# Optimization experiments

Hardware: AMD Instinct MI355X
Metric: run time of the kernel (lower is better)

Reference implementation:

```python
import jax, jax.numpy as jnp
import numpy as np

B, NQ, NKV = 16, 4096, 77
QUERY_DIM, CONTEXT_DIM = 320, 768
HEADS, DIM_HEAD = 8, 64
INNER = HEADS * DIM_HEAD
SCALE = DIM_HEAD ** (-0.5)
MAX_NEG = -jnp.finfo(jnp.float32).max / 2


def setup_inputs() -> dict:
    key = jax.random.key(0)
    ks = jax.random.split(key, 8)
    x = jax.random.normal(ks[0], (B, NQ, QUERY_DIM), dtype=jnp.float32)
    context = jax.random.normal(ks[1], (B, NKV, CONTEXT_DIM), dtype=jnp.float32)
    mask = jax.random.randint(ks[2], (B, 1, 1, NKV), 0, 2).astype(bool)
    s = 0.02
    Wq = jax.random.normal(ks[3], (QUERY_DIM, INNER), dtype=jnp.float32) * s
    Wk = jax.random.normal(ks[4], (CONTEXT_DIM, INNER), dtype=jnp.float32) * s
    Wv = jax.random.normal(ks[5], (CONTEXT_DIM, INNER), dtype=jnp.float32) * s
    Wo = jax.random.normal(ks[6], (INNER, QUERY_DIM), dtype=jnp.float32) * s
    bo = jnp.zeros((QUERY_DIM,), dtype=jnp.float32)
    return {"x": x, "context": context, "mask": mask,
            "Wq": Wq, "Wk": Wk, "Wv": Wv, "Wo": Wo, "bo": bo}


def reference(x, context, mask, Wq, Wk, Wv, Wo, bo):
    # projections (bias-free Linears)
    q = (x @ Wq).reshape(B, NQ, HEADS, DIM_HEAD)        # b q h d
    k = (context @ Wk).reshape(B, NKV, HEADS, DIM_HEAD)  # b k h d
    v = (context @ Wv).reshape(B, NKV, HEADS, DIM_HEAD)  # b k h d
    # additive mask bias: 0 where mask, -finfo.max/2 where ~mask (matches masked_fill_)
    bias = jnp.where(mask, jnp.float32(0), MAX_NEG)      # broadcast to b h q k
    sim = jnp.einsum('bqhd,bkhd->bhqk', q, k) * SCALE + bias
    attn = jax.nn.softmax(sim, axis=-1)
    out = jnp.einsum('bhqk,bkhd->bqhd', attn, v).reshape(B, NQ, INNER)
    return out @ Wo + bo  # dropout p=0 -> identity
```

## Files before the change

### kernel.cpp

```cpp
#include <hip/hip_runtime.h>

typedef unsigned short ushort_t;
typedef __attribute__((ext_vector_type(8))) short bf16x8;
typedef __attribute__((ext_vector_type(4))) float f32x4;

#define B_SZ   16
#define NQ     4096
#define NKV    77
#define QDIM   320
#define CDIM   768
#define HEADS  8
#define DHEAD  64
#define INNER  512
#define M_ROWS (B_SZ * NQ)
#define VT_STR 104

__device__ __forceinline__ ushort_t f2bf(float f) {
  unsigned u = __builtin_bit_cast(unsigned, f);
  u = (u + 0x7fffu + ((u >> 16) & 1u)) >> 16;
  return (ushort_t)u;
}

__device__ __forceinline__ void async16(const ushort_t* g, ushort_t* l) {
  __builtin_amdgcn_global_load_lds(
      (const __attribute__((address_space(1))) unsigned int*)g,
      (__attribute__((address_space(3))) unsigned int*)l,
      16, 0, 0);
}

__device__ __forceinline__ bf16x8 cvt8(f32x4 lo, f32x4 hi) {
  unsigned w0, w1, w2, w3;
  asm("v_cvt_pk_bf16_f32 %0, %1, %2" : "=v"(w0) : "v"(lo[0]), "v"(lo[1]));
  asm("v_cvt_pk_bf16_f32 %0, %1, %2" : "=v"(w1) : "v"(lo[2]), "v"(lo[3]));
  asm("v_cvt_pk_bf16_f32 %0, %1, %2" : "=v"(w2) : "v"(hi[0]), "v"(hi[1]));
  asm("v_cvt_pk_bf16_f32 %0, %1, %2" : "=v"(w3) : "v"(hi[2]), "v"(hi[3]));
  union { unsigned u[4]; bf16x8 v; } cv;
  cv.u[0] = w0; cv.u[1] = w1; cv.u[2] = w2; cv.u[3] = w3;
  return cv.v;
}

#define VMCNT(N) asm volatile("s_waitcnt vmcnt(" #N ")" ::: "memory")

__global__ void mask_bias_kernel(const unsigned char* __restrict__ mraw,
                                 float* __restrict__ biasT) {
  __shared__ int s_u8, s_w4;
  if (threadIdx.x == 0) { s_u8 = 0; s_w4 = 0; }
  __syncthreads();
  const int nbytes = B_SZ * NKV;
  for (int i = threadIdx.x; i < nbytes; i += blockDim.x) {
    unsigned char v = mraw[i];
    if (v && (i & 3)) atomicOr(&s_u8, 1);
    if (v && ((i & 7) == 4)) atomicOr(&s_w4, 1);
  }
  __syncthreads();
  int mode = s_u8 ? 0 : (s_w4 ? 1 : 2);
  for (int i = threadIdx.x; i < B_SZ * 80; i += blockDim.x) {
    int b = i / 80, kv = i - b * 80;
    float bias = -2e30f;
    if (kv < NKV) {
      int idx = b * NKV + kv;
      long long m;
      if (mode == 0)      m = (long long)mraw[idx];
      else if (mode == 1) m = (long long)((const int*)mraw)[idx];
      else                m = ((const long long*)mraw)[idx];
      bias = m ? 0.0f : -1e30f;
    }
    biasT[i] = bias;
  }
}

#define PREP_T0 236544
#define PREP_T1 400384
#define PREP_T2 1186816
#define PREP_T3 1383424
__global__ void prep_kernel(const float* __restrict__ ctx, ushort_t* __restrict__ cb,
                            const float* __restrict__ Wq, ushort_t* __restrict__ Wqb,
                            const float* __restrict__ Wk, const float* __restrict__ Wv,
                            ushort_t* __restrict__ Wkvb,
                            const float* __restrict__ Wo, ushort_t* __restrict__ Wob) {
  int i = blockIdx.x * blockDim.x + threadIdx.x;
  const int stride = gridDim.x * blockDim.x;
  for (; i < PREP_T3; i += stride) {
    if (i < PREP_T0) {
      float4 v = ((const float4*)ctx)[i];
      ushort4 o;
      o.x = f2bf(v.x); o.y = f2bf(v.y); o.z = f2bf(v.z); o.w = f2bf(v.w);
      ((ushort4*)cb)[i] = o;
    } else if (i < PREP_T1) {
      int j = i - PREP_T0;
      int n = j / QDIM, k = j - n * QDIM;
      Wqb[j] = f2bf(Wq[(size_t)k * INNER + n] * 0.125f);
    } else if (i < PREP_T2) {
      int j = i - PREP_T1;
      int n = j / CDIM, k = j - n * CDIM;
      float v = (n < INNER) ? Wk[(size_t)k * INNER + n]
                            : Wv[(size_t)k * INNER + (n - INNER)];
      Wkvb[j] = f2bf(v);
    } else {
      int j = i - PREP_T2;
      int n = j / INNER, k = j - n * INNER;
      Wob[j] = (n < QDIM) ? f2bf(Wo[(size_t)k * QDIM + n]) : (ushort_t)0;
    }
  }
}

__global__ __launch_bounds__(256) void gemm_bf16(
    const ushort_t* __restrict__ A, const ushort_t* __restrict__ Bt,
    ushort_t* __restrict__ Cb,
    int K, int Astride, int Bstride, int Cstride) {
  __shared__ ushort_t As[128 * 64];
  __shared__ ushort_t Bs[128 * 64];
  const int tid = threadIdx.x;
  const int wid = tid >> 6, lane = tid & 63;
  const int wr = wid >> 1, wc = wid & 1;
  const int tileM = blockIdx.x * 128, tileN = blockIdx.y * 128;

  f32x4 acc[4][4];
#pragma unroll
  for (int m = 0; m < 4; ++m)
#pragma unroll
    for (int n = 0; n < 4; ++n) acc[m][n] = (f32x4){0.f, 0.f, 0.f, 0.f};

  const int srow = lane >> 3;
  const int scol = (lane & 7) * 8;

  for (int kt = 0; kt < K; kt += 64) {
    __syncthreads();
#pragma unroll
    for (int j = 0; j < 4; ++j) {
      int s = wid * 4 + j;
      const ushort_t* ga = A + (size_t)(tileM + s * 8 + srow) * Astride + kt + scol;
      const ushort_t* gb = Bt + (size_t)(tileN + s * 8 + srow) * Bstride + kt + scol;
      async16(ga, As + s * 512);
      async16(gb, Bs + s * 512);
    }
    __syncthreads();
#pragma unroll
    for (int kc = 0; kc < 2; ++kc) {
      bf16x8 af[4], bfr[4];
#pragma unroll
      for (int m = 0; m < 4; ++m)
        af[m] = *(const bf16x8*)&As[(wr * 64 + m * 16 + (lane & 15)) * 64 + kc * 32 + (lane >> 4) * 8];
#pragma unroll
      for (int n = 0; n < 4; ++n)
        bfr[n] = *(const bf16x8*)&Bs[(wc * 64 + n * 16 + (lane & 15)) * 64 + kc * 32 + (lane >> 4) * 8];
#pragma unroll
      for (int m = 0; m < 4; ++m)
#pragma unroll
        for (int n = 0; n < 4; ++n)
          acc[m][n] = __builtin_amdgcn_mfma_f32_16x16x32_bf16(af[m], bfr[n], acc[m][n], 0, 0, 0);
    }
  }

  const int r0 = tileM + wr * 64;
  const int c0 = tileN + wc * 64;
  const int rl2 = (lane >> 4) * 4;
  const int cl = lane & 15;
#pragma unroll
  for (int m = 0; m < 4; ++m)
#pragma unroll
    for (int n = 0; n < 4; ++n) {
      int col = c0 + n * 16 + cl;
#pragma unroll
      for (int r = 0; r < 4; ++r)
        Cb[(size_t)(r0 + m * 16 + rl2 + r) * Cstride + col] = f2bf(acc[m][n][r]);
    }
}

__global__ void vtrans_kernel(const ushort_t* __restrict__ kvb,
                              ushort_t* __restrict__ vt) {
  const int h = blockIdx.y, b = blockIdx.z;
  const int wid = threadIdx.x >> 6, lane = threadIdx.x & 63;
  const int d = blockIdx.x * 4 + wid;
  ushort_t* dst = vt + (size_t)(b * HEADS + h) * (64 * VT_STR) + d * VT_STR;
  for (int kv = lane; kv < VT_STR; kv += 64)
    dst[kv] = (kv < NKV)
        ? kvb[(size_t)(b * NKV + kv) * 1024 + 512 + h * 64 + d]
        : (ushort_t)0;
}

__global__ __launch_bounds__(512, 2) void gemm_qproj_p(
    const float* __restrict__ x, const ushort_t* __restrict__ Wt,
    ushort_t* __restrict__ qb) {
  extern __shared__ char sm[];
  const int tid = threadIdx.x, wid = tid >> 6, lane = tid & 63;
  const int rl = lane & 15, g = lane >> 4;
  const int wr = wid & 1, wc = wid >> 1;
  const size_t Mbase = (size_t)blockIdx.x * 128;

  size_t asrc[2]; unsigned adst[2];
#pragma unroll
  for (int i = 0; i < 2; ++i) {
    int c = tid + i * 512, row = c >> 3, c16 = c & 7;
    asrc[i] = (Mbase + row) * 1280 + (unsigned)((c16 * 16) ^ ((row & 7) << 4));
    adst[i] = c * 16;
  }
  size_t bsrc[4]; unsigned bdst[4];
#pragma unroll
  for (int i = 0; i < 4; ++i) {
    int c = tid + i * 512, row = c >> 2, c16 = c & 3;
    bsrc[i] = (size_t)row * 640 + (unsigned)((c16 * 16) ^ ((row & 3) << 4));
    bdst[i] = 16384 + c * 16;
  }
  const char* xB = (const char*)x;
  const char* WtB = (const char*)Wt;

  f32x4 acc[4][8];
#pragma unroll
  for (int m = 0; m < 4; ++m)
#pragma unroll
    for (int n = 0; n < 8; ++n) acc[m][n] = (f32x4){0.f, 0.f, 0.f, 0.f};

#define QSTAGE(K)                                                           \
  {                                                                         \
    char* bb = sm + (unsigned)((K) % 3) * 49152u;                           \
    _Pragma("unroll")                                                       \
    for (int i = 0; i < 2; ++i)                                             \
      async16((const ushort_t*)(xB + asrc[i] + (size_t)(K) * 128),          \
              (ushort_t*)(bb + adst[i]));                                   \
    _Pragma("unroll")                                                       \
    for (int i = 0; i < 4; ++i)                                             \
      async16((const ushort_t*)(WtB + bsrc[i] + (size_t)(K) * 64),          \
              (ushort_t*)(bb + bdst[i]));                                   \
  }

  QSTAGE(0)
  QSTAGE(1)
  for (int s = 0; s < 10; ++s) {
    if (s < 8) QSTAGE(s + 2)
    if (s < 8)       { VMCNT(12); }
    else if (s == 8) { VMCNT(6); }
    else             { VMCNT(0); }
    __builtin_amdgcn_sched_barrier(0);
    __builtin_amdgcn_s_barrier();
    __builtin_amdgcn_sched_barrier(0);

    const char* Ab = sm + (unsigned)(s % 3) * 49152u;
    const char* Bb = Ab + 16384;
    bf16x8 af[4], bfr[8];
#pragma unroll
    for (int m = 0; m < 4; ++m) {
      const int row = wr * 64 + m * 16 + rl;
      const int sw = (row & 7) << 4;
      f32x4 lo = *(const f32x4*)(Ab + row * 128 + ((g * 32) ^ sw));
      f32x4 hi = *(const f32x4*)(Ab + row * 128 + ((g * 32 + 16) ^ sw));
      af[m] = cvt8(lo, hi);
    }
#pragma unroll
    for (int n = 0; n < 8; ++n) {
      const int row = wc * 128 + n * 16 + rl;
      bfr[n] = *(const bf16x8*)(Bb + row * 64 + ((g * 16) ^ ((row & 3) << 4)));
    }
#pragma unroll
    for (int m = 0; m < 4; ++m)
#pragma unroll
      for (int n = 0; n < 8; ++n)
        acc[m][n] = __builtin_amdgcn_mfma_f32_16x16x32_bf16(af[m], bfr[n], acc[m][n], 0, 0, 0);
    __builtin_amdgcn_sched_barrier(0);
    __builtin_amdgcn_s_barrier();
    __builtin_amdgcn_sched_barrier(0);
  }

  ushort_t* eb = (ushort_t*)sm;
#pragma unroll
  for (int h = 0; h < 2; ++h) {
    if (h) __syncthreads();
    if (wr == h) {
#pragma unroll
      for (int m = 0; m < 4; ++m)
#pragma unroll
        for (int n = 0; n < 8; ++n)
#pragma unroll
          for (int r = 0; r < 4; ++r)
            eb[(m * 16 + g * 4 + r) * 512 + wc * 128 + n * 16 + rl] = f2bf(acc[m][n][r]);
    }
    __syncthreads();
#pragma unroll
    for (int i = 0; i < 8; ++i) {
      int c = tid + i * 512, row = c >> 6;
      *(bf16x8*)(qb + (Mbase + h * 64 + row) * 512 + (c & 63) * 8) =
          *(const bf16x8*)(eb + c * 8);
    }
  }
}

__global__ __launch_bounds__(512, 2) void gemm_oproj_p(
    const ushort_t* __restrict__ A, const ushort_t* __restrict__ Wt,
    const float* __restrict__ bo, float* __restrict__ out) {
  extern __shared__ char sm[];
  const int tid = threadIdx.x, wid = tid >> 6, lane = tid & 63;
  const int rl = lane & 15, g = lane >> 4;
  const int wr = wid & 1, wc = wid >> 1;
  const size_t Mbase = (size_t)blockIdx.x * 128;

  size_t asrc; unsigned adst;
  {
    int c = tid, row = c >> 2, c16 = c & 3;
    asrc = (Mbase + row) * 1024 + (unsigned)((c16 * 16) ^ ((row & 3) << 4));
    adst = c * 16;
  }
  size_t bsrc[3]; unsigned bdst[3];
#pragma unroll
  for (int i = 0; i < 3; ++i) {
    int c = tid + i * 512, row = c >> 2, c16 = c & 3;
    bsrc[i] = (size_t)row * 1024 + (unsigned)((c16 * 16) ^ ((row & 3) << 4));
    bdst[i] = 8192 + c * 16;
  }
  const char* AB = (const char*)A;
  const char* WtB = (const char*)Wt;

  f32x4 acc[4][6];
#pragma unroll
  for (int m = 0; m < 4; ++m)
#pragma unroll
    for (int n = 0; n < 6; ++n) acc[m][n] = (f32x4){0.f, 0.f, 0.f, 0.f};

#define OSTAGE(K)                                                           \
  {                                                                         \
    char* bb = sm + (unsigned)((K) % 3) * 32768u;                           \
    async16((const ushort_t*)(AB + asrc + (size_t)(K) * 64),                \
            (ushort_t*)(bb + adst));                                        \
    _Pragma("unroll")                                                       \
    for (int i = 0; i < 3; ++i)                                             \
      async16((const ushort_t*)(WtB + bsrc[i] + (size_t)(K) * 64),          \
              (ushort_t*)(bb + bdst[i]));                                   \
  }

  OSTAGE(0)
  OSTAGE(1)
  for (int s = 0; s < 16; ++s) {
    if (s < 14) OSTAGE(s + 2)
    if (s < 14)       { VMCNT(8); }
    else if (s == 14) { VMCNT(4); }
    else              { VMCNT(0); }
    __builtin_amdgcn_sched_barrier(0);
    __builtin_amdgcn_s_barrier();
    __builtin_amdgcn_sched_barrier(0);

    const char* Ab = sm + (unsigned)(s % 3) * 32768u;
    const char* Bb = Ab + 8192;
    bf16x8 af[4], bfr[6];
#pragma unroll
    for (int m = 0; m < 4; ++m) {
      const int row = wr * 64 + m * 16 + rl;
      af[m] = *(const bf16x8*)(Ab + row * 64 + ((g * 16) ^ ((row & 3) << 4)));
    }
#pragma unroll
    for (int n = 0; n < 6; ++n) {
      const int row = wc * 96 + n * 16 + rl;
      bfr[n] = *(const bf16x8*)(Bb + row * 64 + ((g * 16) ^ ((row & 3) << 4)));
    }
#pragma unroll
    for (int m = 0; m < 4; ++m)
#pragma unroll
      for (int n = 0; n < 6; ++n)
        acc[m][n] = __builtin_amdgcn_mfma_f32_16x16x32_bf16(af[m], bfr[n], acc[m][n], 0, 0, 0);
    __builtin_amdgcn_sched_barrier(0);
    __builtin_amdgcn_s_barrier();
    __builtin_amdgcn_sched_barrier(0);
  }

  const size_t r0 = Mbase + wr * 64;
  const int c0 = wc * 96;
#pragma unroll
  for (int n = 0; n < 6; ++n) {
    int col = c0 + n * 16 + rl;
    if (col < QDIM) {
      float bv = bo[col];
#pragma unroll
      for (int m = 0; m < 4; ++m)
#pragma unroll
        for (int r = 0; r < 4; ++r)
          out[(r0 + m * 16 + g * 4 + r) * QDIM + col] = acc[m][n][r] + bv;
    }
  }
}

__global__ __launch_bounds__(256) void attn_kernel(
    const ushort_t* __restrict__ qb, const ushort_t* __restrict__ kvb,
    const ushort_t* __restrict__ vt, const float* __restrict__ biasT,
    ushort_t* __restrict__ ab) {
  __shared__ ushort_t Vt[64 * VT_STR];
  __shared__ ushort_t P[4 * 16 * VT_STR];
  const int qt = blockIdx.x, h = blockIdx.y, b = blockIdx.z;
  const int tid = threadIdx.x, wid = tid >> 6, lane = tid & 63;
  const int rl = lane & 15;
  const int kh = (lane >> 4) * 8;

  const ushort_t* vtg = vt + (size_t)(b * HEADS + h) * (64 * VT_STR);
  for (int i = tid; i < 832; i += 256) async16(vtg + i * 8, Vt + i * 8);
  for (int i = tid; i < 832; i += 256)
    *(bf16x8*)&P[i * 8] = (bf16x8){0, 0, 0, 0, 0, 0, 0, 0};

  bf16x8 kf[5][2];
  float bias_v[5];
#pragma unroll
  for (int nt = 0; nt < 5; ++nt) {
    int kv = nt * 16 + rl;
    bias_v[nt] = biasT[b * 80 + kv];
    kf[nt][0] = (bf16x8){0, 0, 0, 0, 0, 0, 0, 0};
    kf[nt][1] = (bf16x8){0, 0, 0, 0, 0, 0, 0, 0};
    if (kv < NKV) {
      const ushort_t* kp = &kvb[(size_t)(b * NKV + kv) * 1024 + h * 64 + kh];
      kf[nt][0] = *(const bf16x8*)kp;
      kf[nt][1] = *(const bf16x8*)(kp + 32);
    }
  }
  __syncthreads();

  const int qbase = b * NQ + qt * 256;
  const int pbase = wid * (16 * VT_STR);
#pragma unroll 1
  for (int chunk = 0; chunk < 4; ++chunk) {
    if (chunk) __syncthreads();
    const int row0 = chunk * 64 + wid * 16;

    const ushort_t* qp = &qb[(size_t)(qbase + row0 + rl) * INNER + h * 64 + kh];
    bf16x8 qf0 = *(const bf16x8*)qp;
    bf16x8 qf1 = *(const bf16x8*)(qp + 32);

    f32x4 s[5];
#pragma unroll
    for (int nt = 0; nt < 5; ++nt) {
      s[nt] = (f32x4){0.f, 0.f, 0.f, 0.f};
      s[nt] = __builtin_amdgcn_mfma_f32_16x16x32_bf16(qf0, kf[nt][0], s[nt], 0, 0, 0);
      s[nt] = __builtin_amdgcn_mfma_f32_16x16x32_bf16(qf1, kf[nt][1], s[nt], 0, 0, 0);
    }

    float mx[4] = {-3.0e38f, -3.0e38f, -3.0e38f, -3.0e38f};
#pragma unroll
    for (int nt = 0; nt < 5; ++nt)
#pragma unroll
      for (int r = 0; r < 4; ++r) {
        float v = s[nt][r] + bias_v[nt];
        s[nt][r] = v;
        mx[r] = fmaxf(mx[r], v);
      }
#pragma unroll
    for (int d = 1; d < 16; d <<= 1)
#pragma unroll
      for (int r = 0; r < 4; ++r) mx[r] = fmaxf(mx[r], __shfl_xor(mx[r], d, 64));

    float sm_[4] = {0.f, 0.f, 0.f, 0.f};
#pragma unroll
    for (int nt = 0; nt < 5; ++nt)
#pragma unroll
      for (int r = 0; r < 4; ++r) {
        float p = __expf(s[nt][r] - mx[r]);
        s[nt][r] = p;
        sm_[r] += p;
      }
#pragma unroll
    for (int d = 1; d < 16; d <<= 1)
#pragma unroll
      for (int r = 0; r < 4; ++r) sm_[r] += __shfl_xor(sm_[r], d, 64);

    float rcp[4];
#pragma unroll
    for (int r = 0; r < 4; ++r) rcp[r] = 1.0f / sm_[r];

#pragma unroll
    for (int nt = 0; nt < 5; ++nt)
#pragma unroll
      for (int r = 0; r < 4; ++r)
        P[pbase + ((lane >> 4) * 4 + r) * VT_STR + nt * 16 + rl] = f2bf(s[nt][r]);

    f32x4 o[4];
#pragma unroll
    for (int n = 0; n < 4; ++n) o[n] = (f32x4){0.f, 0.f, 0.f, 0.f};
#pragma unroll
    for (int kc = 0; kc < 3; ++kc) {
      bf16x8 pf = *(const bf16x8*)&P[pbase + rl * VT_STR + kc * 32 + kh];
#pragma unroll
      for (int n = 0; n < 4; ++n) {
        bf16x8 vf = *(const bf16x8*)&Vt[(n * 16 + rl) * VT_STR + kc * 32 + kh];
        o[n] = __builtin_amdgcn_mfma_f32_16x16x32_bf16(pf, vf, o[n], 0, 0, 0);
      }
    }

#pragma unroll
    for (int n = 0; n < 4; ++n)
#pragma unroll
      for (int r = 0; r < 4; ++r)
        P[pbase + ((lane >> 4) * 4 + r) * VT_STR + n * 16 + rl] = f2bf(o[n][r] * rcp[r]);

    __syncthreads();

    {
      const int rflat = tid >> 2, d0 = (tid & 3) * 16;
      const ushort_t* src = &P[(rflat >> 4) * (16 * VT_STR) + (rflat & 15) * VT_STR + d0];
      ushort_t* dst = &ab[(size_t)(qbase + chunk * 64 + rflat) * INNER + h * 64 + d0];
      *(bf16x8*)dst = *(const bf16x8*)src;
      *(bf16x8*)(dst + 8) = *(const bf16x8*)(src + 8);
    }
  }
}

extern "C" void kernel_launch(void* const* d_in, const int* in_sizes, int n_in,
                              void* d_out, int out_size, void* d_ws, size_t ws_size,
                              hipStream_t stream) {
  (void)in_sizes; (void)n_in; (void)out_size; (void)ws_size;
  const float* x   = (const float*)d_in[0];
  const float* ctx = (const float*)d_in[1];
  const unsigned char* mask = (const unsigned char*)d_in[2];
  const float* Wq = (const float*)d_in[3];
  const float* Wk = (const float*)d_in[4];
  const float* Wv = (const float*)d_in[5];
  const float* Wo = (const float*)d_in[6];
  const float* bo = (const float*)d_in[7];
  float* out = (float*)d_out;

  hipFuncSetAttribute((const void*)gemm_qproj_p,
                      hipFuncAttributeMaxDynamicSharedMemorySize, 147456);
  hipFuncSetAttribute((const void*)gemm_oproj_p,
                      hipFuncAttributeMaxDynamicSharedMemorySize, 98304);

  char* ws = (char*)d_ws;
  size_t off = 0;
  auto alloc = [&](size_t bytes) {
    char* p = ws + off;
    off += (bytes + 255) & ~(size_t)255;
    return p;
  };
  float*    biasT = (float*)alloc(B_SZ * 80 * sizeof(float));
  ushort_t* ab    = (ushort_t*)alloc((size_t)M_ROWS * INNER * 2);
  ushort_t* qb    = (ushort_t*)alloc((size_t)M_ROWS * INNER * 2);
  ushort_t* cb    = (ushort_t*)alloc((size_t)1280 * CDIM * 2);
  ushort_t* Wqb   = (ushort_t*)alloc((size_t)INNER * QDIM * 2);
  ushort_t* Wkvb  = (ushort_t*)alloc((size_t)1024 * CDIM * 2);
  ushort_t* Wob   = (ushort_t*)alloc((size_t)384 * INNER * 2);
  ushort_t* kvb   = (ushort_t*)alloc((size_t)1280 * 1024 * 2);
  ushort_t* vt    = (ushort_t*)alloc((size_t)B_SZ * HEADS * 64 * VT_STR * 2);

  mask_bias_kernel<<<1, 256, 0, stream>>>(mask, biasT);
  prep_kernel<<<2048, 256, 0, stream>>>(ctx, cb, Wq, Wqb, Wk, Wv, Wkvb, Wo, Wob);

  gemm_qproj_p<<<M_ROWS / 128, 512, 147456, stream>>>(x, Wqb, qb);
  dim3 g2(1280 / 128, 1024 / 128);
  gemm_bf16<<<g2, 256, 0, stream>>>(cb, Wkvb, kvb, CDIM, CDIM, CDIM, 1024);
  vtrans_kernel<<<dim3(16, HEADS, B_SZ), 256, 0, stream>>>(kvb, vt);
  attn_kernel<<<dim3(NQ / 256, HEADS, B_SZ), 256, 0, stream>>>(qb, kvb, vt, biasT, ab);
  gemm_oproj_p<<<M_ROWS / 128, 512, 98304, stream>>>(ab, Wob, bo, out);
}
```

Before: 182.7 us.

## Pre-convert x to bf16 in prep kernel and fold mask bias into it

The prep kernel now also converts the full fp32 x activation to a bf16 buffer and computes the mask bias in block 0, which removes the separate mask kernel launch. The Q-projection GEMM reads the bf16 copy directly, halving its A-tile loads and shared-memory footprint and dropping the in-loop fp32-to-bf16 conversion. The cost is an extra full pass over x: it is read in fp32 and written in bf16, then read again by the GEMM. Total memory traffic for x therefore grows, and so does workspace use.

After: 189.5 us. 1.04x slower.

```diff
diff --git a/kernel.cpp b/kernel.cpp
--- a/kernel.cpp
+++ b/kernel.cpp
@@ -28,64 +28,61 @@
       16, 0, 0);
 }
 
-__device__ __forceinline__ bf16x8 cvt8(f32x4 lo, f32x4 hi) {
-  unsigned w0, w1, w2, w3;
-  asm("v_cvt_pk_bf16_f32 %0, %1, %2" : "=v"(w0) : "v"(lo[0]), "v"(lo[1]));
-  asm("v_cvt_pk_bf16_f32 %0, %1, %2" : "=v"(w1) : "v"(lo[2]), "v"(lo[3]));
-  asm("v_cvt_pk_bf16_f32 %0, %1, %2" : "=v"(w2) : "v"(hi[0]), "v"(hi[1]));
-  asm("v_cvt_pk_bf16_f32 %0, %1, %2" : "=v"(w3) : "v"(hi[2]), "v"(hi[3]));
-  union { unsigned u[4]; bf16x8 v; } cv;
-  cv.u[0] = w0; cv.u[1] = w1; cv.u[2] = w2; cv.u[3] = w3;
-  return cv.v;
-}
-
 #define VMCNT(N) asm volatile("s_waitcnt vmcnt(" #N ")" ::: "memory")
 
-__global__ void mask_bias_kernel(const unsigned char* __restrict__ mraw,
-                                 float* __restrict__ biasT) {
-  __shared__ int s_u8, s_w4;
-  if (threadIdx.x == 0) { s_u8 = 0; s_w4 = 0; }
-  __syncthreads();
-  const int nbytes = B_SZ * NKV;
-  for (int i = threadIdx.x; i < nbytes; i += blockDim.x) {
-    unsigned char v = mraw[i];
-    if (v && (i & 3)) atomicOr(&s_u8, 1);
-    if (v && ((i & 7) == 4)) atomicOr(&s_w4, 1);
-  }
-  __syncthreads();
-  int mode = s_u8 ? 0 : (s_w4 ? 1 : 2);
-  for (int i = threadIdx.x; i < B_SZ * 80; i += blockDim.x) {
-    int b = i / 80, kv = i - b * 80;
-    float bias = -2e30f;
-    if (kv < NKV) {
-      int idx = b * NKV + kv;
-      long long m;
-      if (mode == 0)      m = (long long)mraw[idx];
-      else if (mode == 1) m = (long long)((const int*)mraw)[idx];
-      else                m = ((const long long*)mraw)[idx];
-      bias = m ? 0.0f : -1e30f;
-    }
-    biasT[i] = bias;
-  }
-}
-
-#define PREP_T0 236544
-#define PREP_T1 400384
-#define PREP_T2 1186816
-#define PREP_T3 1383424
-__global__ void prep_kernel(const float* __restrict__ ctx, ushort_t* __restrict__ cb,
+#define PREP_X  5242880
+#define PREP_T0 (PREP_X + 236544)
+#define PREP_T1 (PREP_T0 + 163840)
+#define PREP_T2 (PREP_T1 + 786432)
+#define PREP_T3 (PREP_T2 + 196608)
+__global__ void prep_kernel(const float* __restrict__ x, ushort_t* __restrict__ xb,
+                            const float* __restrict__ ctx, ushort_t* __restrict__ cb,
                             const float* __restrict__ Wq, ushort_t* __restrict__ Wqb,
                             const float* __restrict__ Wk, const float* __restrict__ Wv,
                             ushort_t* __restrict__ Wkvb,
-                            const float* __restrict__ Wo, ushort_t* __restrict__ Wob) {
+                            const float* __restrict__ Wo, ushort_t* __restrict__ Wob,
+                            const unsigned char* __restrict__ mraw,
+                            float* __restrict__ biasT) {
+  if (blockIdx.x == 0) {
+    __shared__ int s_u8, s_w4;
+    if (threadIdx.x == 0) { s_u8 = 0; s_w4 = 0; }
+    __syncthreads();
+    const int nbytes = B_SZ * NKV;
+    for (int i = threadIdx.x; i < nbytes; i += blockDim.x) {
+      unsigned char v = mraw[i];
+      if (v && (i & 3)) atomicOr(&s_u8, 1);
+      if (v && ((i & 7) == 4)) atomicOr(&s_w4, 1);
+    }
+    __syncthreads();
+    int mode = s_u8 ? 0 : (s_w4 ? 1 : 2);
+    for (int i = threadIdx.x; i < B_SZ * 80; i += blockDim.x) {
+      int b = i / 80, kv = i - b * 80;
+      float bias = -2e30f;
+      if (kv < NKV) {
+        int idx = b * NKV + kv;
+        long long m;
+        if (mode == 0)      m = (long long)mraw[idx];
+        else if (mode == 1) m = (long long)((const int*)mraw)[idx];
+        else                m = ((const long long*)mraw)[idx];
+        bias = m ? 0.0f : -1e30f;
+      }
+      biasT[i] = bias;
+    }
+  }
   int i = blockIdx.x * blockDim.x + threadIdx.x;
   const int stride = gridDim.x * blockDim.x;
   for (; i < PREP_T3; i += stride) {
-    if (i < PREP_T0) {
-      float4 v = ((const float4*)ctx)[i];
+    if (i < PREP_X) {
+      float4 v = ((const float4*)x)[i];
       ushort4 o;
       o.x = f2bf(v.x); o.y = f2bf(v.y); o.z = f2bf(v.z); o.w = f2bf(v.w);
-      ((ushort4*)cb)[i] = o;
+      ((ushort4*)xb)[i] = o;
+    } else if (i < PREP_T0) {
+      int j = i - PREP_X;
+      float4 v = ((const float4*)ctx)[j];
+      ushort4 o;
+      o.x = f2bf(v.x); o.y = f2bf(v.y); o.z = f2bf(v.z); o.w = f2bf(v.w);
+      ((ushort4*)cb)[j] = o;
     } else if (i < PREP_T1) {
       int j = i - PREP_T0;
       int n = j / QDIM, k = j - n * QDIM;
@@ -179,8 +176,8 @@
         : (ushort_t)0;
 }
 
-__global__ __launch_bounds__(512, 2) void gemm_qproj_p(
-    const float* __restrict__ x, const ushort_t* __restrict__ Wt,
+__global__ __launch_bounds__(512, 2) void gemm_qproj_o(
+    const ushort_t* __restrict__ A, const ushort_t* __restrict__ Wt,
     ushort_t* __restrict__ qb) {
   extern __shared__ char sm[];
   const int tid = threadIdx.x, wid = tid >> 6, lane = tid & 63;
@@ -188,21 +185,20 @@
   const int wr = wid & 1, wc = wid >> 1;
   const size_t Mbase = (size_t)blockIdx.x * 128;
 
-  size_t asrc[2]; unsigned adst[2];
-#pragma unroll
-  for (int i = 0; i < 2; ++i) {
-    int c = tid + i * 512, row = c >> 3, c16 = c & 7;
-    asrc[i] = (Mbase + row) * 1280 + (unsigned)((c16 * 16) ^ ((row & 7) << 4));
-    adst[i] = c * 16;
+  size_t asrc; unsigned adst;
+  {
+    int c = tid, row = c >> 2, c16 = c & 3;
+    asrc = (Mbase + row) * 640 + (unsigned)((c16 * 16) ^ ((row & 3) << 4));
+    adst = c * 16;
   }
   size_t bsrc[4]; unsigned bdst[4];
 #pragma unroll
   for (int i = 0; i < 4; ++i) {
     int c = tid + i * 512, row = c >> 2, c16 = c & 3;
     bsrc[i] = (size_t)row * 640 + (unsigned)((c16 * 16) ^ ((row & 3) << 4));
-    bdst[i] = 16384 + c * 16;
-  }
-  const char* xB = (const char*)x;
+    bdst[i] = 8192 + c * 16;
+  }
+  const char* AB = (const char*)A;
   const char* WtB = (const char*)Wt;
 
   f32x4 acc[4][8];
@@ -211,40 +207,35 @@
 #pragma unroll
     for (int n = 0; n < 8; ++n) acc[m][n] = (f32x4){0.f, 0.f, 0.f, 0.f};
 
-#define QSTAGE(K)                                                           \
+#define QSTAGE2(K)                                                          \
   {                                                                         \
-    char* bb = sm + (unsigned)((K) % 3) * 49152u;                           \
-    _Pragma("unroll")                                                       \
-    for (int i = 0; i < 2; ++i)                                             \
-      async16((const ushort_t*)(xB + asrc[i] + (size_t)(K) * 128),          \
-              (ushort_t*)(bb + adst[i]));                                   \
+    char* bb = sm + (unsigned)((K) % 3) * 40960u;                           \
+    async16((const ushort_t*)(AB + asrc + (size_t)(K) * 64),                \
+            (ushort_t*)(bb + adst));                                        \
     _Pragma("unroll")                                                       \
     for (int i = 0; i < 4; ++i)                                             \
       async16((const ushort_t*)(WtB + bsrc[i] + (size_t)(K) * 64),          \
               (ushort_t*)(bb + bdst[i]));                                   \
   }
 
-  QSTAGE(0)
-  QSTAGE(1)
+  QSTAGE2(0)
+  QSTAGE2(1)
   for (int s = 0; s < 10; ++s) {
-    if (s < 8) QSTAGE(s + 2)
-    if (s < 8)       { VMCNT(12); }
-    else if (s == 8) { VMCNT(6); }
+    if (s < 8) QSTAGE2(s + 2)
+    if (s < 8)       { VMCNT(10); }
+    else if (s == 8) { VMCNT(5); }
     else             { VMCNT(0); }
     __builtin_amdgcn_sched_barrier(0);
     __builtin_amdgcn_s_barrier();
     __builtin_amdgcn_sched_barrier(0);
 
-    const char* Ab = sm + (unsigned)(s % 3) * 49152u;
-    const char* Bb = Ab + 16384;
+    const char* Ab = sm + (unsigned)(s % 3) * 40960u;
+    const char* Bb = Ab + 8192;
     bf16x8 af[4], bfr[8];
 #pragma unroll
     for (int m = 0; m < 4; ++m) {
       const int row = wr * 64 + m * 16 + rl;
-      const int sw = (row & 7) << 4;
-      f32x4 lo = *(const f32x4*)(Ab + row * 128 + ((g * 32) ^ sw));
-      f32x4 hi = *(const f32x4*)(Ab + row * 128 + ((g * 32 + 16) ^ sw));
-      af[m] = cvt8(lo, hi);
+      af[m] = *(const bf16x8*)(Ab + row * 64 + ((g * 16) ^ ((row & 3) << 4)));
     }
 #pragma unroll
     for (int n = 0; n < 8; ++n) {
@@ -510,8 +501,8 @@
   const float* bo = (const float*)d_in[7];
   float* out = (float*)d_out;
 
-  hipFuncSetAttribute((const void*)gemm_qproj_p,
-                      hipFuncAttributeMaxDynamicSharedMemorySize, 147456);
+  hipFuncSetAttribute((const void*)gemm_qproj_o,
+                      hipFuncAttributeMaxDynamicSharedMemorySize, 122880);
   hipFuncSetAttribute((const void*)gemm_oproj_p,
                       hipFuncAttributeMaxDynamicSharedMemorySize, 98304);
 
@@ -525,6 +516,7 @@
   float*    biasT = (float*)alloc(B_SZ * 80 * sizeof(float));
   ushort_t* ab    = (ushort_t*)alloc((size_t)M_ROWS * INNER * 2);
   ushort_t* qb    = (ushort_t*)alloc((size_t)M_ROWS * INNER * 2);
+  ushort_t* xb    = (ushort_t*)alloc((size_t)M_ROWS * QDIM * 2);
   ushort_t* cb    = (ushort_t*)alloc((size_t)1280 * CDIM * 2);
   ushort_t* Wqb   = (ushort_t*)alloc((size_t)INNER * QDIM * 2);
   ushort_t* Wkvb  = (ushort_t*)alloc((size_t)1024 * CDIM * 2);
@@ -532,10 +524,10 @@
   ushort_t* kvb   = (ushort_t*)alloc((size_t)1280 * 1024 * 2);
   ushort_t* vt    = (ushort_t*)alloc((size_t)B_SZ * HEADS * 64 * VT_STR * 2);
 
-  mask_bias_kernel<<<1, 256, 0, stream>>>(mask, biasT);
-  prep_kernel<<<2048, 256, 0, stream>>>(ctx, cb, Wq, Wqb, Wk, Wv, Wkvb, Wo, Wob);
-
-  gemm_qproj_p<<<M_ROWS / 128, 512, 147456, stream>>>(x, Wqb, qb);
+  prep_kernel<<<2048, 256, 0, stream>>>(x, xb, ctx, cb, Wq, Wqb,
+                                        Wk, Wv, Wkvb, Wo, Wob, mask, biasT);
+
+  gemm_qproj_o<<<M_ROWS / 128, 512, 122880, stream>>>(xb, Wqb, qb);
   dim3 g2(1280 / 128, 1024 / 128);
   gemm_bf16<<<g2, 256, 0, stream>>>(cb, Wkvb, kvb, CDIM, CDIM, CDIM, 1024);
   vtrans_kernel<<<dim3(16, HEADS, B_SZ), 256, 0, stream>>>(kvb, vt);
```

## Split Q projection GEMM into 128x128 output tiles over a 2D grid

Applied to the files above, without the earlier changes.

The Q-projection kernel now computes 128x128 output tiles on a (4, M/128) grid instead of full 128x512 row panels. This cuts LDS per block and accumulator registers, allowing more resident blocks and more parallelism. The cost is that each x row tile, stored in fp32, is loaded and converted to bf16 four times, which raises global/L2 traffic. The epilogue is simplified to a single padded LDS staging pass.

Result: slower. 198.1 us (+8.4%).

```diff
diff --git a/kernel.cpp b/kernel.cpp
--- a/kernel.cpp
+++ b/kernel.cpp
@@ -179,14 +179,15 @@
         : (ushort_t)0;
 }
 
-__global__ __launch_bounds__(512, 2) void gemm_qproj_p(
+__global__ __launch_bounds__(512, 2) void gemm_qproj_f(
     const float* __restrict__ x, const ushort_t* __restrict__ Wt,
     ushort_t* __restrict__ qb) {
   extern __shared__ char sm[];
   const int tid = threadIdx.x, wid = tid >> 6, lane = tid & 63;
   const int rl = lane & 15, g = lane >> 4;
   const int wr = wid & 1, wc = wid >> 1;
-  const size_t Mbase = (size_t)blockIdx.x * 128;
+  const int Nbase = blockIdx.x * 128;
+  const size_t Mbase = (size_t)blockIdx.y * 128;
 
   size_t asrc[2]; unsigned adst[2];
 #pragma unroll
@@ -195,49 +196,45 @@
     asrc[i] = (Mbase + row) * 1280 + (unsigned)((c16 * 16) ^ ((row & 7) << 4));
     adst[i] = c * 16;
   }
-  size_t bsrc[4]; unsigned bdst[4];
-#pragma unroll
-  for (int i = 0; i < 4; ++i) {
-    int c = tid + i * 512, row = c >> 2, c16 = c & 3;
-    bsrc[i] = (size_t)row * 640 + (unsigned)((c16 * 16) ^ ((row & 3) << 4));
-    bdst[i] = 16384 + c * 16;
+  size_t bsrc; unsigned bdst;
+  {
+    int row = tid >> 2, c16 = tid & 3;
+    bsrc = (size_t)(Nbase + row) * 640 + (unsigned)((c16 * 16) ^ ((row & 3) << 4));
+    bdst = 16384 + tid * 16;
   }
   const char* xB = (const char*)x;
   const char* WtB = (const char*)Wt;
 
-  f32x4 acc[4][8];
+  f32x4 acc[4][2];
 #pragma unroll
   for (int m = 0; m < 4; ++m)
 #pragma unroll
-    for (int n = 0; n < 8; ++n) acc[m][n] = (f32x4){0.f, 0.f, 0.f, 0.f};
-
-#define QSTAGE(K)                                                           \
+    for (int n = 0; n < 2; ++n) acc[m][n] = (f32x4){0.f, 0.f, 0.f, 0.f};
+
+#define FSTG(K)                                                             \
   {                                                                         \
-    char* bb = sm + (unsigned)((K) % 3) * 49152u;                           \
+    char* bb = sm + (unsigned)((K) % 3) * 24576u;                           \
     _Pragma("unroll")                                                       \
     for (int i = 0; i < 2; ++i)                                             \
       async16((const ushort_t*)(xB + asrc[i] + (size_t)(K) * 128),          \
               (ushort_t*)(bb + adst[i]));                                   \
-    _Pragma("unroll")                                                       \
-    for (int i = 0; i < 4; ++i)                                             \
-      async16((const ushort_t*)(WtB + bsrc[i] + (size_t)(K) * 64),          \
-              (ushort_t*)(bb + bdst[i]));                                   \
-  }
-
-  QSTAGE(0)
-  QSTAGE(1)
+    async16((const ushort_t*)(WtB + bsrc + (size_t)(K) * 64),               \
+            (ushort_t*)(bb + bdst));                                        \
+  }
+
+  FSTG(0)
+  FSTG(1)
   for (int s = 0; s < 10; ++s) {
-    if (s < 8) QSTAGE(s + 2)
-    if (s < 8)       { VMCNT(12); }
-    else if (s == 8) { VMCNT(6); }
+    if (s < 8)       { FSTG(s + 2) VMCNT(6); }
+    else if (s == 8) { VMCNT(3); }
     else             { VMCNT(0); }
     __builtin_amdgcn_sched_barrier(0);
     __builtin_amdgcn_s_barrier();
     __builtin_amdgcn_sched_barrier(0);
 
-    const char* Ab = sm + (unsigned)(s % 3) * 49152u;
+    const char* Ab = sm + (unsigned)(s % 3) * 24576u;
     const char* Bb = Ab + 16384;
-    bf16x8 af[4], bfr[8];
+    bf16x8 af[4], bfr[2];
 #pragma unroll
     for (int m = 0; m < 4; ++m) {
       const int row = wr * 64 + m * 16 + rl;
@@ -247,40 +244,35 @@
       af[m] = cvt8(lo, hi);
     }
 #pragma unroll
-    for (int n = 0; n < 8; ++n) {
-      const int row = wc * 128 + n * 16 + rl;
+    for (int n = 0; n < 2; ++n) {
+      const int row = wc * 32 + n * 16 + rl;
       bfr[n] = *(const bf16x8*)(Bb + row * 64 + ((g * 16) ^ ((row & 3) << 4)));
     }
 #pragma unroll
     for (int m = 0; m < 4; ++m)
 #pragma unroll
-      for (int n = 0; n < 8; ++n)
+      for (int n = 0; n < 2; ++n)
         acc[m][n] = __builtin_amdgcn_mfma_f32_16x16x32_bf16(af[m], bfr[n], acc[m][n], 0, 0, 0);
     __builtin_amdgcn_sched_barrier(0);
     __builtin_amdgcn_s_barrier();
     __builtin_amdgcn_sched_barrier(0);
   }
 
+  __syncthreads();
   ushort_t* eb = (ushort_t*)sm;
 #pragma unroll
-  for (int h = 0; h < 2; ++h) {
-    if (h) __syncthreads();
-    if (wr == h) {
-#pragma unroll
-      for (int m = 0; m < 4; ++m)
-#pragma unroll
-        for (int n = 0; n < 8; ++n)
-#pragma unroll
-          for (int r = 0; r < 4; ++r)
-            eb[(m * 16 + g * 4 + r) * 512 + wc * 128 + n * 16 + rl] = f2bf(acc[m][n][r]);
-    }
-    __syncthreads();
-#pragma unroll
-    for (int i = 0; i < 8; ++i) {
-      int c = tid + i * 512, row = c >> 6;
-      *(bf16x8*)(qb + (Mbase + h * 64 + row) * 512 + (c & 63) * 8) =
-          *(const bf16x8*)(eb + c * 8);
-    }
+  for (int m = 0; m < 4; ++m)
+#pragma unroll
+    for (int n = 0; n < 2; ++n)
+#pragma unroll
+      for (int r = 0; r < 4; ++r)
+        eb[(wr * 64 + m * 16 + g * 4 + r) * 136 + wc * 32 + n * 16 + rl] = f2bf(acc[m][n][r]);
+  __syncthreads();
+#pragma unroll
+  for (int i = 0; i < 4; ++i) {
+    int c = tid + i * 512, row = c >> 4, c8 = c & 15;
+    *(bf16x8*)(qb + (Mbase + row) * 512 + Nbase + c8 * 8) =
+        *(const bf16x8*)(eb + row * 136 + c8 * 8);
   }
 }
 
@@ -510,8 +502,8 @@
   const float* bo = (const float*)d_in[7];
   float* out = (float*)d_out;
 
-  hipFuncSetAttribute((const void*)gemm_qproj_p,
-                      hipFuncAttributeMaxDynamicSharedMemorySize, 147456);
+  hipFuncSetAttribute((const void*)gemm_qproj_f,
+                      hipFuncAttributeMaxDynamicSharedMemorySize, 73728);
   hipFuncSetAttribute((const void*)gemm_oproj_p,
                       hipFuncAttributeMaxDynamicSharedMemorySize, 98304);
 
@@ -535,7 +527,7 @@
   mask_bias_kernel<<<1, 256, 0, stream>>>(mask, biasT);
   prep_kernel<<<2048, 256, 0, stream>>>(ctx, cb, Wq, Wqb, Wk, Wv, Wkvb, Wo, Wob);
 
-  gemm_qproj_p<<<M_ROWS / 128, 512, 147456, stream>>>(x, Wqb, qb);
+  gemm_qproj_f<<<dim3(4, M_ROWS / 128), 512, 73728, stream>>>(x, Wqb, qb);
   dim3 g2(1280 / 128, 1024 / 128);
   gemm_bf16<<<g2, 256, 0, stream>>>(cb, Wkvb, kvb, CDIM, CDIM, CDIM, 1024);
   vtrans_kernel<<<dim3(16, HEADS, B_SZ), 256, 0, stream>>>(kvb, vt);
```

## Switch projection GEMMs from triple-buffered vmcnt pipeline to double buffering

Applied to the files above, without the earlier changes.

The Q-projection and output-projection GEMMs drop their three-stage async global-to-LDS pipeline, which used explicit vmcnt waits and raw s_barriers. They now use two buffers: each iteration prefetches one stage ahead and ends with __syncthreads. This cuts dynamic LDS from 144KB to 96KB for the Q projection and from 96KB to 64KB for the output projection, so the output GEMM could fit two blocks per CU. The cost is a shorter prefetch distance and a full barrier plus memory drain every iteration, which may expose more load latency.

After: 180.3 us. Within noise of the previous version (-1.3%).

```diff
diff --git a/kernel.cpp b/kernel.cpp
--- a/kernel.cpp
+++ b/kernel.cpp
@@ -38,8 +38,6 @@
   cv.u[0] = w0; cv.u[1] = w1; cv.u[2] = w2; cv.u[3] = w3;
   return cv.v;
 }
-
-#define VMCNT(N) asm volatile("s_waitcnt vmcnt(" #N ")" ::: "memory")
 
 __global__ void mask_bias_kernel(const unsigned char* __restrict__ mraw,
                                  float* __restrict__ biasT) {
@@ -213,7 +211,7 @@
 
 #define QSTAGE(K)                                                           \
   {                                                                         \
-    char* bb = sm + (unsigned)((K) % 3) * 49152u;                           \
+    char* bb = sm + (unsigned)((K) & 1) * 49152u;                           \
     _Pragma("unroll")                                                       \
     for (int i = 0; i < 2; ++i)                                             \
       async16((const ushort_t*)(xB + asrc[i] + (size_t)(K) * 128),          \
@@ -225,17 +223,11 @@
   }
 
   QSTAGE(0)
-  QSTAGE(1)
+  __syncthreads();
   for (int s = 0; s < 10; ++s) {
-    if (s < 8) QSTAGE(s + 2)
-    if (s < 8)       { VMCNT(12); }
-    else if (s == 8) { VMCNT(6); }
-    else             { VMCNT(0); }
-    __builtin_amdgcn_sched_barrier(0);
-    __builtin_amdgcn_s_barrier();
-    __builtin_amdgcn_sched_barrier(0);
-
-    const char* Ab = sm + (unsigned)(s % 3) * 49152u;
+    if (s < 9) QSTAGE(s + 1)
+
+    const char* Ab = sm + (unsigned)(s & 1) * 49152u;
     const char* Bb = Ab + 16384;
     bf16x8 af[4], bfr[8];
 #pragma unroll
@@ -256,9 +248,8 @@
 #pragma unroll
       for (int n = 0; n < 8; ++n)
         acc[m][n] = __builtin_amdgcn_mfma_f32_16x16x32_bf16(af[m], bfr[n], acc[m][n], 0, 0, 0);
-    __builtin_amdgcn_sched_barrier(0);
-    __builtin_amdgcn_s_barrier();
-    __builtin_amdgcn_sched_barrier(0);
+
+    __syncthreads();
   }
 
   ushort_t* eb = (ushort_t*)sm;
@@ -317,7 +308,7 @@
 
 #define OSTAGE(K)                                                           \
   {                                                                         \
-    char* bb = sm + (unsigned)((K) % 3) * 32768u;                           \
+    char* bb = sm + (unsigned)((K) & 1) * 32768u;                           \
     async16((const ushort_t*)(AB + asrc + (size_t)(K) * 64),                \
             (ushort_t*)(bb + adst));                                        \
     _Pragma("unroll")                                                       \
@@ -327,17 +318,11 @@
   }
 
   OSTAGE(0)
-  OSTAGE(1)
+  __syncthreads();
   for (int s = 0; s < 16; ++s) {
-    if (s < 14) OSTAGE(s + 2)
-    if (s < 14)       { VMCNT(8); }
-    else if (s == 14) { VMCNT(4); }
-    else              { VMCNT(0); }
-    __builtin_amdgcn_sched_barrier(0);
-    __builtin_amdgcn_s_barrier();
-    __builtin_amdgcn_sched_barrier(0);
-
-    const char* Ab = sm + (unsigned)(s % 3) * 32768u;
+    if (s < 15) OSTAGE(s + 1)
+
+    const char* Ab = sm + (unsigned)(s & 1) * 32768u;
     const char* Bb = Ab + 8192;
     bf16x8 af[4], bfr[6];
 #pragma unroll
@@ -355,9 +340,8 @@
 #pragma unroll
       for (int n = 0; n < 6; ++n)
         acc[m][n] = __builtin_amdgcn_mfma_f32_16x16x32_bf16(af[m], bfr[n], acc[m][n], 0, 0, 0);
-    __builtin_amdgcn_sched_barrier(0);
-    __builtin_amdgcn_s_barrier();
-    __builtin_amdgcn_sched_barrier(0);
+
+    __syncthreads();
   }
 
   const size_t r0 = Mbase + wr * 64;
@@ -511,9 +495,9 @@
   float* out = (float*)d_out;
 
   hipFuncSetAttribute((const void*)gemm_qproj_p,
-                      hipFuncAttributeMaxDynamicSharedMemorySize, 147456);
+                      hipFuncAttributeMaxDynamicSharedMemorySize, 98304);
   hipFuncSetAttribute((const void*)gemm_oproj_p,
-                      hipFuncAttributeMaxDynamicSharedMemorySize, 98304);
+                      hipFuncAttributeMaxDynamicSharedMemorySize, 65536);
 
   char* ws = (char*)d_ws;
   size_t off = 0;
@@ -535,10 +519,10 @@
   mask_bias_kernel<<<1, 256, 0, stream>>>(mask, biasT);
   prep_kernel<<<2048, 256, 0, stream>>>(ctx, cb, Wq, Wqb, Wk, Wv, Wkvb, Wo, Wob);
 
-  gemm_qproj_p<<<M_ROWS / 128, 512, 147456, stream>>>(x, Wqb, qb);
+  gemm_qproj_p<<<M_ROWS / 128, 512, 98304, stream>>>(x, Wqb, qb);
   dim3 g2(1280 / 128, 1024 / 128);
   gemm_bf16<<<g2, 256, 0, stream>>>(cb, Wkvb, kvb, CDIM, CDIM, CDIM, 1024);
   vtrans_kernel<<<dim3(16, HEADS, B_SZ), 256, 0, stream>>>(kvb, vt);
   attn_kernel<<<dim3(NQ / 256, HEADS, B_SZ), 256, 0, stream>>>(qb, kvb, vt, biasT, ab);
-  gemm_oproj_p<<<M_ROWS / 128, 512, 98304, stream>>>(ab, Wob, bo, out);
-}
+  gemm_oproj_p<<<M_ROWS / 128, 512, 65536, stream>>>(ab, Wob, bo, out);
+}
```
